# Performance work log

Hardware: AMD Instinct MI355X
Metric: run time of the kernel (lower is better)

The kernel has to match this reference:

```python
import jax, jax.numpy as jnp
import numpy as np

# Adaptive-LIF constants (Yin et al. spiking RNN, which this thesis repo builds on)
B_J0 = 0.01    # baseline threshold
BETA = 1.8     # adaptation strength
GAMMA = 0.5    # surrogate gradient scale
LENS = 0.5     # surrogate gaussian width
HIGHT = 0.15   # multi-gaussian side-lobe height
SCALE = 6.0    # side-lobe width multiplier


def _gaussian(x, mu, sigma):
    return jnp.exp(-((x - mu) ** 2) / (2.0 * sigma ** 2)) / (jnp.sqrt(2.0 * jnp.pi) * sigma)


@jax.custom_vjp
def spike_fn(v):
    # Heaviside spike with multi-gaussian surrogate gradient
    return (v > 0).astype(v.dtype)

def _spike_fwd(v):
    return spike_fn(v), v

def _spike_bwd(v, g):
    sg = (_gaussian(v, 0.0, LENS) * (1.0 + HIGHT)
          - _gaussian(v, LENS, SCALE * LENS) * HIGHT
          - _gaussian(v, -LENS, SCALE * LENS) * HIGHT)
    return (g * sg * GAMMA,)

spike_fn.defvjp(_spike_fwd, _spike_bwd)


def setup_inputs() -> dict:
    key = jax.random.key(0)
    ks = jax.random.split(key, 16)
    B, S, C, H, O = 256, 250, 700, 256, 20

    def lin(k, fan_in, shape):  # nn.Linear default init
        lim = 1.0 / np.sqrt(fan_in)
        return jax.random.uniform(k, shape, jnp.float32, -lim, lim)

    def tau(k, mean, std, shape):
        return jnp.clip(mean + std * jax.random.normal(k, shape, jnp.float32), 1.0, None)

    return {
        "x": jax.random.normal(ks[0], (B, S, C), jnp.float32),
        # forward spiking cell (tauM ~ N(20, ~5), tauAdp ~ N(200, ~50))
        "W_in_f": lin(ks[1], C, (C, H)), "b_in_f": lin(ks[2], C, (H,)),
        "W_rec_f": lin(ks[3], H, (H, H)), "b_rec_f": lin(ks[4], H, (H,)),
        "tau_m_f": tau(ks[5], 20.0, 5.0, (H,)),
        "tau_adp_f": tau(ks[6], 200.0, 50.0, (H,)),
        # backward spiking cell
        "W_in_b": lin(ks[7], C, (C, H)), "b_in_b": lin(ks[8], C, (H,)),
        "W_rec_b": lin(ks[9], H, (H, H)), "b_rec_b": lin(ks[10], H, (H,)),
        "tau_m_b": tau(ks[11], 20.0, 5.0, (H,)),
        "tau_adp_b": tau(ks[12], 200.0, 50.0, (H,)),
        # readout leaky integrator over concat(fw, bw) = 512 -> 20, tauM ~ N(3, 1)
        "W_out": lin(ks[13], 2 * H, (2 * H, O)), "b_out": lin(ks[14], 2 * H, (O,)),
        "tau_m_out": tau(ks[15], 3.0, 1.0, (O,)),
    }


def reference(x, W_in_f, b_in_f, W_rec_f, b_rec_f, tau_m_f, tau_adp_f,
              W_in_b, b_in_b, W_rec_b, b_rec_b, tau_m_b, tau_adp_b,
              W_out, b_out, tau_m_out):
    B, S, C = x.shape
    H = W_in_f.shape[1]
    O = W_out.shape[1]

    alpha_f = jnp.exp(-1.0 / tau_m_f); ro_f = jnp.exp(-1.0 / tau_adp_f)
    alpha_b = jnp.exp(-1.0 / tau_m_b); ro_b = jnp.exp(-1.0 / tau_adp_b)
    alpha_o = jnp.exp(-1.0 / tau_m_out)

    # Batch the feed-forward input projections over all timesteps: [S, B, H]
    proj_f = jnp.einsum("bsc,ch->sbh", x, W_in_f) + b_in_f
    proj_b = jnp.einsum("bsc,ch->sbh", x[:, ::-1], W_in_b) + b_in_b

    def cell(in_t, mem, spk, bb, W_rec, b_rec, alpha, ro):
        # mem_update_adp: adaptive threshold LIF
        d = in_t + spk @ W_rec + b_rec
        bb = ro * bb + (1.0 - ro) * spk
        thr = B_J0 + BETA * bb
        mem = mem * alpha + (1.0 - alpha) * d - thr * spk
        spk = spike_fn(mem - thr)
        return mem, spk, bb

    def step(carry, xs):
        mem_f, spk_f, bb_f, mem_b, spk_b, bb_b, mem_o = carry
        in_f, in_b = xs
        mem_f, spk_f, bb_f = cell(in_f, mem_f, spk_f, bb_f, W_rec_f, b_rec_f, alpha_f, ro_f)
        mem_b, spk_b, bb_b = cell(in_b, mem_b, spk_b, bb_b, W_rec_b, b_rec_b, alpha_b, ro_b)
        # readout integrator over concat(fw, bw) spikes (method=1 integrates every step)
        merged = jnp.concatenate([spk_f, spk_b], axis=-1)
        mem_o = mem_o * alpha_o + (1.0 - alpha_o) * (merged @ W_out + b_out)
        return (mem_f, spk_f, bb_f, mem_b, spk_b, bb_b, mem_o), None

    z = jnp.zeros((B, H), x.dtype)
    b0 = jnp.full((B, H), B_J0, x.dtype)
    carry0 = (z, z, b0, z, z, b0, jnp.zeros((B, O), x.dtype))
    carry, _ = jax.lax.scan(step, carry0, (proj_f, proj_b))
    return jax.nn.log_softmax(carry[-1], axis=-1)
```

## Files before the change

kernel.cpp:

```cpp
#include <hip/hip_runtime.h>
#include <cstdint>
#include <cstddef>

#define S_LEN 250
#define BATCH 256
#define CIN   700
#define HID   256
#define OUT_N 20
#define KSTEPS 22

typedef __attribute__((ext_vector_type(8))) short bf16x8;
typedef __attribute__((ext_vector_type(4))) float f32x4;

__device__ __forceinline__ ushort f2bf_rne(float f) {
    uint u = __float_as_uint(f);
    uint r = (u + 0x7FFFu + ((u >> 16) & 1u)) >> 16;
    return (ushort)r;
}
__device__ __forceinline__ float bf2f(ushort h) {
    return __uint_as_float(((uint)h) << 16);
}

__global__ __launch_bounds__(256) void proj_mfma(
    const float* __restrict__ x,
    const float* __restrict__ Wf, const float* __restrict__ Wb,
    const float* __restrict__ biasf, const float* __restrict__ biasb,
    float* __restrict__ P)
{
    __shared__ ushort AsH[128][40];
    __shared__ ushort AsL[128][40];
    __shared__ ushort BsH[128][40];
    __shared__ ushort BsL[128][40];

    const int nt = blockIdx.x;
    const int mt = blockIdx.y;
    const int m0 = mt * 128;
    const float* W   = (nt < 2) ? Wf : Wb;
    const float* bia = (nt < 2) ? biasf : biasb;
    const int wc0 = (nt & 1) * 128;

    const int tid  = threadIdx.x;
    const int lane = tid & 63;
    const int wv   = tid >> 6;
    const int wr   = wv >> 1;
    const int wc   = wv & 1;
    const int l15  = lane & 15;
    const int l4   = lane >> 4;

    const int as  = tid & 7;
    const int arr = tid >> 3;
    const int bcol = tid & 127;
    const int bkh  = tid >> 7;

    f32x4 acc[4][4];
#pragma unroll
    for (int i = 0; i < 4; i++)
#pragma unroll
        for (int j = 0; j < 4; j++)
            acc[i][j] = (f32x4){0.f, 0.f, 0.f, 0.f};

    float4 av[4];
    float bv[16];

#define PROJ_LOAD(K0_) do {                                                   \
        const int ka_ = (K0_) + as * 4;                                       \
        const bool aok_ = (ka_ + 3) < CIN;                                    \
        _Pragma("unroll")                                                     \
        for (int i_ = 0; i_ < 4; i_++) {                                      \
            av[i_] = make_float4(0.f, 0.f, 0.f, 0.f);                         \
            if (aok_)                                                         \
                av[i_] = *(const float4*)&x[(size_t)(m0 + arr + 32 * i_) * CIN + ka_]; \
        }                                                                     \
        _Pragma("unroll")                                                     \
        for (int j_ = 0; j_ < 16; j_++) {                                     \
            const int kb_ = (K0_) + bkh * 16 + j_;                            \
            bv[j_] = (kb_ < CIN) ? W[(size_t)kb_ * HID + wc0 + bcol] : 0.f;   \
        }                                                                     \
    } while (0)

#define PROJ_CVT_WRITE() do {                                                 \
        _Pragma("unroll")                                                     \
        for (int i_ = 0; i_ < 4; i_++) {                                      \
            const int row_ = arr + 32 * i_;                                   \
            ushort4 h_, l_;                                                   \
            h_.x = f2bf_rne(av[i_].x); l_.x = f2bf_rne(__fsub_rn(av[i_].x, bf2f(h_.x))); \
            h_.y = f2bf_rne(av[i_].y); l_.y = f2bf_rne(__fsub_rn(av[i_].y, bf2f(h_.y))); \
            h_.z = f2bf_rne(av[i_].z); l_.z = f2bf_rne(__fsub_rn(av[i_].z, bf2f(h_.z))); \
            h_.w = f2bf_rne(av[i_].w); l_.w = f2bf_rne(__fsub_rn(av[i_].w, bf2f(h_.w))); \
            *(ushort4*)&AsH[row_][as * 4] = h_;                               \
            *(ushort4*)&AsL[row_][as * 4] = l_;                               \
        }                                                                     \
        _Pragma("unroll")                                                     \
        for (int q_ = 0; q_ < 4; q_++) {                                      \
            ushort4 h_, l_;                                                   \
            float v0_ = bv[q_ * 4 + 0], v1_ = bv[q_ * 4 + 1];                 \
            float v2_ = bv[q_ * 4 + 2], v3_ = bv[q_ * 4 + 3];                 \
            h_.x = f2bf_rne(v0_); l_.x = f2bf_rne(__fsub_rn(v0_, bf2f(h_.x))); \
            h_.y = f2bf_rne(v1_); l_.y = f2bf_rne(__fsub_rn(v1_, bf2f(h_.y))); \
            h_.z = f2bf_rne(v2_); l_.z = f2bf_rne(__fsub_rn(v2_, bf2f(h_.z))); \
            h_.w = f2bf_rne(v3_); l_.w = f2bf_rne(__fsub_rn(v3_, bf2f(h_.w))); \
            *(ushort4*)&BsH[bcol][bkh * 16 + q_ * 4] = h_;                    \
            *(ushort4*)&BsL[bcol][bkh * 16 + q_ * 4] = l_;                    \
        }                                                                     \
    } while (0)

    PROJ_LOAD(0);
    PROJ_CVT_WRITE();

    for (int kt = 0; kt < KSTEPS; kt++) {
        __syncthreads();
        if (kt + 1 < KSTEPS)
            PROJ_LOAD((kt + 1) * 32);

#pragma unroll
        for (int fc = 0; fc < 4; fc++) {
            const bf16x8 bHf = *(const bf16x8*)&BsH[wc * 64 + fc * 16 + l15][l4 * 8];
            const bf16x8 bLf = *(const bf16x8*)&BsL[wc * 64 + fc * 16 + l15][l4 * 8];
#pragma unroll
            for (int fr = 0; fr < 4; fr++) {
                const bf16x8 aHf = *(const bf16x8*)&AsH[wr * 64 + fr * 16 + l15][l4 * 8];
                const bf16x8 aLf = *(const bf16x8*)&AsL[wr * 64 + fr * 16 + l15][l4 * 8];
                acc[fr][fc] = __builtin_amdgcn_mfma_f32_16x16x32_bf16(
                    aHf, bHf, acc[fr][fc], 0, 0, 0);
                acc[fr][fc] = __builtin_amdgcn_mfma_f32_16x16x32_bf16(
                    aHf, bLf, acc[fr][fc], 0, 0, 0);
                acc[fr][fc] = __builtin_amdgcn_mfma_f32_16x16x32_bf16(
                    aLf, bHf, acc[fr][fc], 0, 0, 0);
            }
        }

        __syncthreads();
        if (kt + 1 < KSTEPS)
            PROJ_CVT_WRITE();
    }

#undef PROJ_LOAD
#undef PROJ_CVT_WRITE

#pragma unroll
    for (int fc = 0; fc < 4; fc++) {
        const float bvs = bia[wc0 + wc * 64 + fc * 16 + l15];
#pragma unroll
        for (int fr = 0; fr < 4; fr++) {
#pragma unroll
            for (int j = 0; j < 4; j++) {
                const int row = m0 + wr * 64 + fr * 16 + l4 * 4 + j;
                P[(size_t)row * 512 + nt * 128 + wc * 64 + fc * 16 + l15] =
                    __fadd_rn(acc[fr][fc][j], bvs);
            }
        }
    }
}

__global__ __launch_bounds__(512, 2) void scan_mfma(
    const float* __restrict__ P,
    const float* __restrict__ Wrecf, const float* __restrict__ brecf,
    const float* __restrict__ taumf, const float* __restrict__ tauaf,
    const float* __restrict__ Wrecb, const float* __restrict__ brecb,
    const float* __restrict__ taumb, const float* __restrict__ tauab,
    const float* __restrict__ Wout, const float* __restrict__ taumo,
    float* __restrict__ Pst)
{
    const int g  = blockIdx.x;
    const int d  = blockIdx.y;
    const int b0 = g * 16;
    const bool fw = (d == 0);

    const int tid  = threadIdx.x;
    const int lane = tid & 63;
    const int w    = tid >> 6;
    const int l15  = lane & 15;
    const int l4   = lane >> 4;

    __shared__ ushort Sp[2][16][264];

    {
        ushort* p = &Sp[0][0][0];
        for (int i = tid; i < 2 * 16 * 264; i += 512) p[i] = 0;
    }

    const float* Wrec = fw ? Wrecf : Wrecb;

    bf16x8 whf[8][2], wlf[8][2];
#pragma unroll
    for (int kt = 0; kt < 8; kt++)
#pragma unroll
        for (int ct = 0; ct < 2; ct++) {
            const int c = w * 32 + ct * 16 + l15;
#pragma unroll
            for (int j = 0; j < 8; j++) {
                const float v = Wrec[(size_t)(kt * 32 + l4 * 8 + j) * HID + c];
                const ushort h = f2bf_rne(v);
                const ushort l = f2bf_rne(__fsub_rn(v, bf2f(h)));
                whf[kt][ct][j] = (short)h;
                wlf[kt][ct][j] = (short)l;
            }
        }

    bf16x8 woh[2], wol[2];
#pragma unroll
    for (int t = 0; t < 2; t++) {
        const int o = t * 16 + l15;
#pragma unroll
        for (int j = 0; j < 8; j++) {
            float v = 0.f;
            if (o < OUT_N)
                v = Wout[(size_t)(d * HID + w * 32 + l4 * 8 + j) * OUT_N + o];
            const ushort h = f2bf_rne(v);
            const ushort l = f2bf_rne(__fsub_rn(v, bf2f(h)));
            woh[t][j] = (short)h;
            wol[t][j] = (short)l;
        }
    }

    float alpha_[2], ro_[2], omA_[2], omR_[2], brc_[2];
#pragma unroll
    for (int t = 0; t < 2; t++) {
        const int c = w * 32 + t * 16 + l15;
        alpha_[t] = expf(__fdiv_rn(-1.f, fw ? taumf[c] : taumb[c]));
        ro_[t]    = expf(__fdiv_rn(-1.f, fw ? tauaf[c] : tauab[c]));
        omA_[t]   = __fsub_rn(1.f, alpha_[t]);
        omR_[t]   = __fsub_rn(1.f, ro_[t]);
        brc_[t]   = fw ? brecf[c] : brecb[c];
    }
    float ao_[2], omo_[2];
#pragma unroll
    for (int t = 0; t < 2; t++) {
        const int o = t * 16 + l15;
        if (o < OUT_N) {
            ao_[t]  = expf(__fdiv_rn(-1.f, taumo[o]));
            omo_[t] = __fsub_rn(1.f, ao_[t]);
        } else { ao_[t] = 0.f; omo_[t] = 0.f; }
    }

    float mem[2][4], bbv[2][4], spkv[2][4], z[2][4];
#pragma unroll
    for (int t = 0; t < 2; t++)
#pragma unroll
        for (int j = 0; j < 4; j++) {
            mem[t][j] = 0.f; bbv[t][j] = 0.01f; spkv[t][j] = 0.f; z[t][j] = 0.f;
        }

    float pv[2][4];
    {
        const int srow = fw ? 0 : (S_LEN - 1);
#pragma unroll
        for (int t = 0; t < 2; t++)
#pragma unroll
            for (int j = 0; j < 4; j++)
                pv[t][j] = P[((size_t)(b0 + l4 * 4 + j) * S_LEN + srow) * 512
                             + d * HID + w * 32 + t * 16 + l15];
    }

    for (int s = 0; s < S_LEN; s++) {
        const int cur = s & 1, prev = cur ^ 1;

        __syncthreads();

        float pv_next[2][4];
        {
            const int sn   = (s + 1 < S_LEN) ? s + 1 : S_LEN - 1;
            const int srow = fw ? sn : (S_LEN - 1 - sn);
#pragma unroll
            for (int t = 0; t < 2; t++)
#pragma unroll
                for (int j = 0; j < 4; j++)
                    pv_next[t][j] = P[((size_t)(b0 + l4 * 4 + j) * S_LEN + srow) * 512
                                      + d * HID + w * 32 + t * 16 + l15];
        }

        f32x4 acc[2];
        acc[0] = (f32x4){0.f, 0.f, 0.f, 0.f};
        acc[1] = (f32x4){0.f, 0.f, 0.f, 0.f};
#pragma unroll
        for (int kt = 0; kt < 8; kt++) {
            const bf16x8 a = *(const bf16x8*)&Sp[prev][l15][kt * 32 + l4 * 8];
            acc[0] = __builtin_amdgcn_mfma_f32_16x16x32_bf16(a, whf[kt][0], acc[0], 0, 0, 0);
            acc[0] = __builtin_amdgcn_mfma_f32_16x16x32_bf16(a, wlf[kt][0], acc[0], 0, 0, 0);
            acc[1] = __builtin_amdgcn_mfma_f32_16x16x32_bf16(a, whf[kt][1], acc[1], 0, 0, 0);
            acc[1] = __builtin_amdgcn_mfma_f32_16x16x32_bf16(a, wlf[kt][1], acc[1], 0, 0, 0);
        }

#pragma unroll
        for (int t = 0; t < 2; t++) {
#pragma unroll
            for (int j = 0; j < 4; j++) {
                const float dd = __fadd_rn(__fadd_rn(pv[t][j], acc[t][j]), brc_[t]);
                bbv[t][j] = __fadd_rn(__fmul_rn(ro_[t], bbv[t][j]),
                                      __fmul_rn(omR_[t], spkv[t][j]));
                const float thr = __fadd_rn(0.01f, __fmul_rn(1.8f, bbv[t][j]));
                mem[t][j] = __fsub_rn(
                    __fadd_rn(__fmul_rn(mem[t][j], alpha_[t]),
                              __fmul_rn(omA_[t], dd)),
                    __fmul_rn(thr, spkv[t][j]));
                const bool sp = __fsub_rn(mem[t][j], thr) > 0.f;
                spkv[t][j] = sp ? 1.f : 0.f;
                Sp[cur][l4 * 4 + j][w * 32 + t * 16 + l15] =
                    sp ? (ushort)0x3F80 : (ushort)0;
            }
        }

        asm volatile("s_waitcnt lgkmcnt(0)" ::: "memory");
        __builtin_amdgcn_sched_barrier(0);

        {
            const bf16x8 ar = *(const bf16x8*)&Sp[cur][l15][w * 32 + l4 * 8];
            f32x4 S0 = (f32x4){0.f, 0.f, 0.f, 0.f};
            f32x4 S1 = (f32x4){0.f, 0.f, 0.f, 0.f};
            S0 = __builtin_amdgcn_mfma_f32_16x16x32_bf16(ar, woh[0], S0, 0, 0, 0);
            S0 = __builtin_amdgcn_mfma_f32_16x16x32_bf16(ar, wol[0], S0, 0, 0, 0);
            S1 = __builtin_amdgcn_mfma_f32_16x16x32_bf16(ar, woh[1], S1, 0, 0, 0);
            S1 = __builtin_amdgcn_mfma_f32_16x16x32_bf16(ar, wol[1], S1, 0, 0, 0);
#pragma unroll
            for (int j = 0; j < 4; j++) {
                z[0][j] = __fmaf_rn(ao_[0], z[0][j], __fmul_rn(omo_[0], S0[j]));
                z[1][j] = __fmaf_rn(ao_[1], z[1][j], __fmul_rn(omo_[1], S1[j]));
            }
        }

#pragma unroll
        for (int t = 0; t < 2; t++)
#pragma unroll
            for (int j = 0; j < 4; j++) pv[t][j] = pv_next[t][j];
    }

    __syncthreads();

    float* stash = Pst + ((size_t)b0 * S_LEN) * 512 + d * HID;
#pragma unroll
    for (int j = 0; j < 4; j++) {
        const int r = l4 * 4 + j;
        const int idx0 = w * 320 + r * 16 + l15;
        stash[(size_t)(idx0 >> 8) * 512 + (idx0 & 255)] = z[0][j];
        if (l15 < 4) {
            const int idx1 = w * 320 + 256 + r * 4 + l15;
            stash[(size_t)(idx1 >> 8) * 512 + (idx1 & 255)] = z[1][j];
        }
    }
}

__global__ __launch_bounds__(64) void merge_out(
    const float* __restrict__ Pst, const float* __restrict__ bout,
    const float* __restrict__ taumo, float* __restrict__ out)
{
    const int bb = blockIdx.x;
    const int o  = threadIdx.x;
    const int g  = bb >> 4, r = bb & 15;

    float val = 0.f, v = -3.0e38f;
    if (o < OUT_N) {
        float tot = 0.f;
#pragma unroll
        for (int d2 = 0; d2 < 2; d2++) {
            const float* stash = Pst + ((size_t)(g * 16) * S_LEN) * 512 + d2 * HID;
#pragma unroll
            for (int w2 = 0; w2 < 8; w2++) {
                const int idx = (o < 16) ? (w2 * 320 + r * 16 + o)
                                         : (w2 * 320 + 256 + r * 4 + (o - 16));
                tot = __fadd_rn(tot, stash[(size_t)(idx >> 8) * 512 + (idx & 255)]);
            }
        }
        const float aS = expf(__fdiv_rn(-(float)S_LEN, taumo[o]));
        val = __fadd_rn(tot, __fmul_rn(bout[o], __fsub_rn(1.f, aS)));
        v = val;
    }
    float mx = v;
#pragma unroll
    for (int d2 = 1; d2 < 64; d2 <<= 1)
        mx = fmaxf(mx, __shfl_xor(mx, d2, 64));
    float e = (o < OUT_N) ? expf(__fsub_rn(val, mx)) : 0.f;
#pragma unroll
    for (int d2 = 1; d2 < 64; d2 <<= 1)
        e += __shfl_xor(e, d2, 64);
    if (o < OUT_N)
        out[(size_t)bb * OUT_N + o] =
            __fsub_rn(__fsub_rn(val, mx), logf(e));
}

extern "C" void kernel_launch(void* const* d_in, const int* in_sizes, int n_in,
                              void* d_out, int out_size, void* d_ws, size_t ws_size,
                              hipStream_t stream) {
    const float* x         = (const float*)d_in[0];
    const float* W_in_f    = (const float*)d_in[1];
    const float* b_in_f    = (const float*)d_in[2];
    const float* W_rec_f   = (const float*)d_in[3];
    const float* b_rec_f   = (const float*)d_in[4];
    const float* tau_m_f   = (const float*)d_in[5];
    const float* tau_adp_f = (const float*)d_in[6];
    const float* W_in_b    = (const float*)d_in[7];
    const float* b_in_b    = (const float*)d_in[8];
    const float* W_rec_b   = (const float*)d_in[9];
    const float* b_rec_b   = (const float*)d_in[10];
    const float* tau_m_b   = (const float*)d_in[11];
    const float* tau_adp_b = (const float*)d_in[12];
    const float* W_out     = (const float*)d_in[13];
    const float* b_out     = (const float*)d_in[14];
    const float* tau_m_o   = (const float*)d_in[15];
    float* out = (float*)d_out;
    float* P   = (float*)d_ws;

    proj_mfma<<<dim3(4, 500), dim3(256), 0, stream>>>(
        x, W_in_f, W_in_b, b_in_f, b_in_b, P);
    scan_mfma<<<dim3(16, 2), dim3(512), 0, stream>>>(
        P, W_rec_f, b_rec_f, tau_m_f, tau_adp_f,
        W_rec_b, b_rec_b, tau_m_b, tau_adp_b,
        W_out, tau_m_o, P);
    merge_out<<<dim3(BATCH), dim3(64), 0, stream>>>(
        P, b_out, tau_m_o, out);
}
```

Baseline: 523.6 us.

## Defer readout MFMA by one step and split recurrent accumulator chains

```diff
diff --git a/kernel.cpp b/kernel.cpp
--- a/kernel.cpp
+++ b/kernel.cpp
@@ -241,87 +241,95 @@
             mem[t][j] = 0.f; bbv[t][j] = 0.01f; spkv[t][j] = 0.f; z[t][j] = 0.f;
         }
 
+    const float* pp0 = P + ((size_t)(b0 + l4 * 4 + 0) * S_LEN + (fw ? 0 : S_LEN - 1)) * 512
+                         + d * HID + w * 32 + l15;
+    const float* pp1 = P + ((size_t)(b0 + l4 * 4 + 1) * S_LEN + (fw ? 0 : S_LEN - 1)) * 512
+                         + d * HID + w * 32 + l15;
+    const float* pp2 = P + ((size_t)(b0 + l4 * 4 + 2) * S_LEN + (fw ? 0 : S_LEN - 1)) * 512
+                         + d * HID + w * 32 + l15;
+    const float* pp3 = P + ((size_t)(b0 + l4 * 4 + 3) * S_LEN + (fw ? 0 : S_LEN - 1)) * 512
+                         + d * HID + w * 32 + l15;
+    const ptrdiff_t pstep = fw ? 512 : -512;
+
     float pv[2][4];
+
+#define SCAN_STEP(CUR, PREV) do {                                              \
+        __syncthreads();   \
+               \
+        pv[0][0] = pp0[0];  pv[1][0] = pp0[16];                                \
+        pv[0][1] = pp1[0];  pv[1][1] = pp1[16];                                \
+        pv[0][2] = pp2[0];  pv[1][2] = pp2[16];                                \
+        pv[0][3] = pp3[0];  pv[1][3] = pp3[16];                                \
+        pp0 += pstep; pp1 += pstep; pp2 += pstep; pp3 += pstep;                \
+        f32x4 accH0 = (f32x4){0.f,0.f,0.f,0.f}, accH1 = (f32x4){0.f,0.f,0.f,0.f}; \
+        f32x4 accL0 = (f32x4){0.f,0.f,0.f,0.f}, accL1 = (f32x4){0.f,0.f,0.f,0.f}; \
+        _Pragma("unroll")                                                      \
+        for (int kt_ = 0; kt_ < 8; kt_++) {                                    \
+            const bf16x8 a_ = *(const bf16x8*)&Sp[PREV][l15][kt_ * 32 + l4 * 8]; \
+            accH0 = __builtin_amdgcn_mfma_f32_16x16x32_bf16(a_, whf[kt_][0], accH0, 0, 0, 0); \
+            accL0 = __builtin_amdgcn_mfma_f32_16x16x32_bf16(a_, wlf[kt_][0], accL0, 0, 0, 0); \
+            accH1 = __builtin_amdgcn_mfma_f32_16x16x32_bf16(a_, whf[kt_][1], accH1, 0, 0, 0); \
+            accL1 = __builtin_amdgcn_mfma_f32_16x16x32_bf16(a_, wlf[kt_][1], accL1, 0, 0, 0); \
+        }                                                                      \
+                 \
+        {                                                                      \
+            const bf16x8 ar_ = *(const bf16x8*)&Sp[PREV][l15][w * 32 + l4 * 8]; \
+            f32x4 S0_ = (f32x4){0.f,0.f,0.f,0.f}, S1_ = (f32x4){0.f,0.f,0.f,0.f}; \
+            S0_ = __builtin_amdgcn_mfma_f32_16x16x32_bf16(ar_, woh[0], S0_, 0, 0, 0); \
+            S0_ = __builtin_amdgcn_mfma_f32_16x16x32_bf16(ar_, wol[0], S0_, 0, 0, 0); \
+            S1_ = __builtin_amdgcn_mfma_f32_16x16x32_bf16(ar_, woh[1], S1_, 0, 0, 0); \
+            S1_ = __builtin_amdgcn_mfma_f32_16x16x32_bf16(ar_, wol[1], S1_, 0, 0, 0); \
+            _Pragma("unroll")                                                  \
+            for (int j_ = 0; j_ < 4; j_++) {                                   \
+                z[0][j_] = __fmaf_rn(ao_[0], z[0][j_], __fmul_rn(omo_[0], S0_[j_])); \
+                z[1][j_] = __fmaf_rn(ao_[1], z[1][j_], __fmul_rn(omo_[1], S1_[j_])); \
+            }                                                                  \
+        }                                                                      \
+                     \
+        _Pragma("unroll")                                                      \
+        for (int t_ = 0; t_ < 2; t_++) {                                       \
+            _Pragma("unroll")                                                  \
+            for (int j_ = 0; j_ < 4; j_++) {                                   \
+                const float accv_ = __fadd_rn((t_ ? accH1 : accH0)[j_],        \
+                                              (t_ ? accL1 : accL0)[j_]);       \
+                const float dd_ = __fadd_rn(__fadd_rn(pv[t_][j_], accv_), brc_[t_]); \
+                bbv[t_][j_] = __fadd_rn(__fmul_rn(ro_[t_], bbv[t_][j_]),       \
+                                        __fmul_rn(omR_[t_], spkv[t_][j_]));    \
+                const float thr_ = __fadd_rn(0.01f, __fmul_rn(1.8f, bbv[t_][j_])); \
+                mem[t_][j_] = __fsub_rn(                                       \
+                    __fadd_rn(__fmul_rn(mem[t_][j_], alpha_[t_]),              \
+                              __fmul_rn(omA_[t_], dd_)),                       \
+                    __fmul_rn(thr_, spkv[t_][j_]));                            \
+                const bool sp_ = __fsub_rn(mem[t_][j_], thr_) > 0.f;           \
+                spkv[t_][j_] = sp_ ? 1.f : 0.f;                                \
+                Sp[CUR][l4 * 4 + j_][w * 32 + t_ * 16 + l15] =                 \
+                    sp_ ? (ushort)0x3F80 : (ushort)0;                          \
+            }                                                                  \
+        }                                                                      \
+    } while (0)
+
+    for (int s2 = 0; s2 < S_LEN / 2; s2++) {
+        SCAN_STEP(0, 1);
+        SCAN_STEP(1, 0);
+    }
+#undef SCAN_STEP
+
+    asm volatile("s_waitcnt lgkmcnt(0)" ::: "memory");
+    __builtin_amdgcn_sched_barrier(0);
+
     {
-        const int srow = fw ? 0 : (S_LEN - 1);
-#pragma unroll
-        for (int t = 0; t < 2; t++)
-#pragma unroll
-            for (int j = 0; j < 4; j++)
-                pv[t][j] = P[((size_t)(b0 + l4 * 4 + j) * S_LEN + srow) * 512
-                             + d * HID + w * 32 + t * 16 + l15];
-    }
-
-    for (int s = 0; s < S_LEN; s++) {
-        const int cur = s & 1, prev = cur ^ 1;
-
-        __syncthreads();
-
-        float pv_next[2][4];
-        {
-            const int sn   = (s + 1 < S_LEN) ? s + 1 : S_LEN - 1;
-            const int srow = fw ? sn : (S_LEN - 1 - sn);
-#pragma unroll
-            for (int t = 0; t < 2; t++)
-#pragma unroll
-                for (int j = 0; j < 4; j++)
-                    pv_next[t][j] = P[((size_t)(b0 + l4 * 4 + j) * S_LEN + srow) * 512
-                                      + d * HID + w * 32 + t * 16 + l15];
-        }
-
-        f32x4 acc[2];
-        acc[0] = (f32x4){0.f, 0.f, 0.f, 0.f};
-        acc[1] = (f32x4){0.f, 0.f, 0.f, 0.f};
-#pragma unroll
-        for (int kt = 0; kt < 8; kt++) {
-            const bf16x8 a = *(const bf16x8*)&Sp[prev][l15][kt * 32 + l4 * 8];
-            acc[0] = __builtin_amdgcn_mfma_f32_16x16x32_bf16(a, whf[kt][0], acc[0], 0, 0, 0);
-            acc[0] = __builtin_amdgcn_mfma_f32_16x16x32_bf16(a, wlf[kt][0], acc[0], 0, 0, 0);
-            acc[1] = __builtin_amdgcn_mfma_f32_16x16x32_bf16(a, whf[kt][1], acc[1], 0, 0, 0);
-            acc[1] = __builtin_amdgcn_mfma_f32_16x16x32_bf16(a, wlf[kt][1], acc[1], 0, 0, 0);
-        }
-
-#pragma unroll
-        for (int t = 0; t < 2; t++) {
-#pragma unroll
-            for (int j = 0; j < 4; j++) {
-                const float dd = __fadd_rn(__fadd_rn(pv[t][j], acc[t][j]), brc_[t]);
-                bbv[t][j] = __fadd_rn(__fmul_rn(ro_[t], bbv[t][j]),
-                                      __fmul_rn(omR_[t], spkv[t][j]));
-                const float thr = __fadd_rn(0.01f, __fmul_rn(1.8f, bbv[t][j]));
-                mem[t][j] = __fsub_rn(
-                    __fadd_rn(__fmul_rn(mem[t][j], alpha_[t]),
-                              __fmul_rn(omA_[t], dd)),
-                    __fmul_rn(thr, spkv[t][j]));
-                const bool sp = __fsub_rn(mem[t][j], thr) > 0.f;
-                spkv[t][j] = sp ? 1.f : 0.f;
-                Sp[cur][l4 * 4 + j][w * 32 + t * 16 + l15] =
-                    sp ? (ushort)0x3F80 : (ushort)0;
-            }
-        }
-
-        asm volatile("s_waitcnt lgkmcnt(0)" ::: "memory");
-        __builtin_amdgcn_sched_barrier(0);
-
-        {
-            const bf16x8 ar = *(const bf16x8*)&Sp[cur][l15][w * 32 + l4 * 8];
-            f32x4 S0 = (f32x4){0.f, 0.f, 0.f, 0.f};
-            f32x4 S1 = (f32x4){0.f, 0.f, 0.f, 0.f};
-            S0 = __builtin_amdgcn_mfma_f32_16x16x32_bf16(ar, woh[0], S0, 0, 0, 0);
-            S0 = __builtin_amdgcn_mfma_f32_16x16x32_bf16(ar, wol[0], S0, 0, 0, 0);
-            S1 = __builtin_amdgcn_mfma_f32_16x16x32_bf16(ar, woh[1], S1, 0, 0, 0);
-            S1 = __builtin_amdgcn_mfma_f32_16x16x32_bf16(ar, wol[1], S1, 0, 0, 0);
-#pragma unroll
-            for (int j = 0; j < 4; j++) {
-                z[0][j] = __fmaf_rn(ao_[0], z[0][j], __fmul_rn(omo_[0], S0[j]));
-                z[1][j] = __fmaf_rn(ao_[1], z[1][j], __fmul_rn(omo_[1], S1[j]));
-            }
-        }
-
-#pragma unroll
-        for (int t = 0; t < 2; t++)
-#pragma unroll
-            for (int j = 0; j < 4; j++) pv[t][j] = pv_next[t][j];
+        const bf16x8 ar = *(const bf16x8*)&Sp[1][l15][w * 32 + l4 * 8];
+        f32x4 S0 = (f32x4){0.f, 0.f, 0.f, 0.f};
+        f32x4 S1 = (f32x4){0.f, 0.f, 0.f, 0.f};
+        S0 = __builtin_amdgcn_mfma_f32_16x16x32_bf16(ar, woh[0], S0, 0, 0, 0);
+        S0 = __builtin_amdgcn_mfma_f32_16x16x32_bf16(ar, wol[0], S0, 0, 0, 0);
+        S1 = __builtin_amdgcn_mfma_f32_16x16x32_bf16(ar, woh[1], S1, 0, 0, 0);
+        S1 = __builtin_amdgcn_mfma_f32_16x16x32_bf16(ar, wol[1], S1, 0, 0, 0);
+#pragma unroll
+        for (int j = 0; j < 4; j++) {
+            z[0][j] = __fmaf_rn(ao_[0], z[0][j], __fmul_rn(omo_[0], S0[j]));
+            z[1][j] = __fmaf_rn(ao_[1], z[1][j], __fmul_rn(omo_[1], S1[j]));
+        }
     }
 
     __syncthreads();
```

After: 622.2 us. 1.19x slower.
